# Kernel optimization log

Hardware: AMD Instinct MI355X
Metric: run time of the kernel (lower is better)

The kernel has to match this reference:

```python
import jax, jax.numpy as jnp
import numpy as np

# Module config (matches init_kwargs)
DIM = 256
NUM_HEADS = 8
KS = (7, 7)            # kernel_sizes per split
DIL = (1, 2)           # dilations per split
NUM_SPLITS = 2
HEADS_PER = NUM_HEADS // NUM_SPLITS  # clean partition: 4 heads per split


def _nb_indices(L, ks, dil):
    """NATTEN neighborhood start + relative-position-bias indices along one axis.
    Each residue class (i % dil) is an independent 1D sequence; the k-window is
    clamped (shifted) at the borders exactly as in NATTEN's get_window_start.
    Returns nb [L, ks] key indices and bi [L, ks] rpb indices in [0, 2ks-2].
    """
    i = jnp.arange(L)
    r = i % dil
    p = i // dil
    Lr = (L - r + dil - 1) // dil              # length of residue class
    ps = jnp.clip(p - ks // 2, 0, Lr - ks)     # window start (subsampled coords)
    a = jnp.arange(ks)
    nb = (ps[:, None] + a[None, :]) * dil + r[:, None]   # [L, ks]
    bi = a[None, :] + (ps - p)[:, None] + (ks - 1)       # [L, ks]
    return nb, bi


def _na_split(q, k, v, rpb, ks, dil):
    """natten2dqkrpb -> softmax -> natten2dav for one head-group.
    q pre-scaled. q/k/v: [B,h,H,W,hd], rpb: [h,2ks-1,2ks-1]."""
    H, W = q.shape[2], q.shape[3]
    hn, hb = _nb_indices(H, ks, dil)
    wn, wb = _nb_indices(W, ks, dil)
    # gather local windows: [B,h,H,W,ks,ks,hd]
    kg = k[:, :, hn[:, None, :, None], wn[None, :, None, :], :]
    vg = v[:, :, hn[:, None, :, None], wn[None, :, None, :], :]
    attn = jnp.einsum('bhijd,bhijkld->bhijkl', q, kg)
    attn = attn + rpb[:, hb[:, None, :, None], wb[None, :, None, :]][None]  # [B,h,H,W,ks,ks]
    B, h = attn.shape[0], attn.shape[1]
    attn = jax.nn.softmax(attn.reshape(B, h, H, W, ks * ks), axis=-1)
    attn = attn.reshape(B, h, H, W, ks, ks)
    return jnp.einsum('bhijkl,bhijkld->bhijd', attn, vg)


def _forward(x, w_qkv, b_qkv, w_proj, b_proj, rpb0, rpb1):
    B, H, W, C = x.shape
    hd = C // NUM_HEADS
    scale = hd ** -0.5
    qkv = (x @ w_qkv + b_qkv).reshape(B, H, W, 3, NUM_HEADS, hd)
    qkv = jnp.transpose(qkv, (3, 0, 4, 1, 2, 5))  # [3,B,nh,H,W,hd]
    q, k, v = qkv[0] * scale, qkv[1], qkv[2]
    outs = []
    for s, rpb in enumerate((rpb0, rpb1)):
        sl = slice(s * HEADS_PER, (s + 1) * HEADS_PER)
        outs.append(_na_split(q[:, sl], k[:, sl], v[:, sl], rpb, KS[s], DIL[s]))
    out = jnp.concatenate(outs, axis=1)                      # [B,nh,H,W,hd]
    out = jnp.transpose(out, (0, 2, 3, 1, 4)).reshape(B, H, W, C)
    return out @ w_proj + b_proj


def setup_inputs() -> dict:
    key = jax.random.key(0)
    ks = jax.random.split(key, 6)
    C = DIM
    x = jax.random.normal(ks[0], (2, 56, 56, C), jnp.float32)
    w_qkv = jax.random.normal(ks[1], (C, 3 * C), jnp.float32) * 0.02
    b_qkv = jnp.zeros((3 * C,), jnp.float32)
    w_proj = jax.random.normal(ks[2], (C, C), jnp.float32) * 0.02
    b_proj = jnp.zeros((C,), jnp.float32)
    rpb0 = jax.random.normal(ks[3], (HEADS_PER, 2 * KS[0] - 1, 2 * KS[0] - 1), jnp.float32) * 0.02
    rpb1 = jax.random.normal(ks[4], (HEADS_PER, 2 * KS[1] - 1, 2 * KS[1] - 1), jnp.float32) * 0.02
    return {'x': x, 'w_qkv': w_qkv, 'b_qkv': b_qkv, 'w_proj': w_proj,
            'b_proj': b_proj, 'rpb0': rpb0, 'rpb1': rpb1}


def reference(x, w_qkv, b_qkv, w_proj, b_proj, rpb0, rpb1):
    return _forward(x, w_qkv, b_qkv, w_proj, b_proj, rpb0, rpb1)
```

## Files before the change

### kernel.cpp

```cpp
#include <hip/hip_runtime.h>
#include <stdint.h>

typedef __bf16 bf16_t;
typedef bf16_t bf16x8 __attribute__((ext_vector_type(8)));
typedef float floatx4 __attribute__((ext_vector_type(4)));

#define HW 56
#define NTOK 6272

__device__ __forceinline__ uint16_t f2bf(float f){
  union { float f; uint32_t i; } c; c.f = f;
  uint32_t r = (c.i + 0x7FFFu + ((c.i >> 16) & 1u)) >> 16;
  return (uint16_t)r;
}
__device__ __forceinline__ float bflo(uint32_t u){
  union { uint32_t i; float f; } c; c.i = u << 16; return c.f;
}
__device__ __forceinline__ float bfhi(uint32_t u){
  union { uint32_t i; float f; } c; c.i = u & 0xffff0000u; return c.f;
}

typedef __attribute__((address_space(1))) const void* gptr_t;
typedef __attribute__((address_space(3))) void* lptr_t;

__global__ __launch_bounds__(256) void prep_kernel(
    const float* __restrict__ x,      uint16_t* __restrict__ xb,
    const float* __restrict__ w_qkv,  uint16_t* __restrict__ wqkvT,
    const float* __restrict__ w_proj, uint16_t* __restrict__ wprojT)
{
  __shared__ uint16_t tile[64][65];
  const int bx = blockIdx.x;
  const int t = threadIdx.x;
  if (bx < 784){
    int idx = bx * 256 + t;
    const float4* s = (const float4*)x + (size_t)idx * 2;
    float4 a = s[0], b = s[1];
    uint4 pk;
    pk.x = (uint32_t)f2bf(a.x) | ((uint32_t)f2bf(a.y) << 16);
    pk.y = (uint32_t)f2bf(a.z) | ((uint32_t)f2bf(a.w) << 16);
    pk.z = (uint32_t)f2bf(b.x) | ((uint32_t)f2bf(b.y) << 16);
    pk.w = (uint32_t)f2bf(b.z) | ((uint32_t)f2bf(b.w) << 16);
    ((uint4*)xb)[idx] = pk;
    return;
  }
  const float* src; uint16_t* dst; int N, q;
  if (bx < 832){ q = bx - 784; src = w_qkv;  dst = wqkvT;  N = 768; }
  else         { q = bx - 832; src = w_proj; dst = wprojT; N = 256; }
  const int k0 = (q & 3) * 64, n0 = (q >> 2) * 64;
  for (int idx = t; idx < 64 * 64; idx += 256){
    int r = idx >> 6, c = idx & 63;
    tile[r][c] = f2bf(src[(k0 + r) * N + n0 + c]);
  }
  __syncthreads();
  for (int idx = t; idx < 64 * 64; idx += 256){
    int r = idx >> 6, c = idx & 63;
    dst[(n0 + r) * 256 + k0 + c] = tile[c][r];
  }
}

#define KDIM 256
#define KHALF 128

template<int OUTF32, int AHM, int NT>
__global__ __launch_bounds__(256) void gemm_bt_bias(
    const uint16_t* __restrict__ A,
    const uint16_t* __restrict__ Bt,
    const float* __restrict__ bias,
    void* __restrict__ Cv,
    int N)
{
  constexpr int NF = NT / 32;
  __shared__ __align__(16) uint16_t Al[64 * KHALF];
  __shared__ __align__(16) uint16_t Bl[NT * KHALF];
  const int m0 = blockIdx.x * 64, n0 = blockIdx.y * NT;
  const int t = threadIdx.x;
  const int lane = t & 63;
  const int wave = t >> 6;
  const int wm = (wave & 1) * 32;
  const int wn = (wave >> 1) * (NF * 16);
  const int fr = lane & 15;
  const int q8 = (lane >> 4) * 8;

  floatx4 acc[2][NF];
  #pragma unroll
  for (int mi = 0; mi < 2; mi++)
    #pragma unroll
    for (int nf = 0; nf < NF; nf++) acc[mi][nf] = (floatx4){0.f,0.f,0.f,0.f};

  constexpr int AGRP = 4;
  constexpr int BGRP = NT / 16;

  for (int ko = 0; ko < 2; ko++){
    if (ko) __syncthreads();
    #pragma unroll
    for (int gg = 0; gg < AGRP; gg++){
      int g = wave + gg * 4;
      int L = g * 64 + lane;
      int row = L >> 4, cs = L & 15;
      int cg = cs ^ (row & 15);
      const uint16_t* ga;
      if (AHM){
        int d0 = ko * KHALF + cg * 8;
        ga = A + (size_t)(d0 >> 5) * (NTOK * 32) + (m0 + row) * 32 + (d0 & 31);
      } else {
        ga = A + (size_t)(m0 + row) * KDIM + ko * KHALF + cg * 8;
      }
      __builtin_amdgcn_global_load_lds((gptr_t)ga, (lptr_t)(Al + g * 512), 16, 0, 0);
    }
    #pragma unroll
    for (int gg = 0; gg < BGRP; gg++){
      int g = wave + gg * 4;
      int L = g * 64 + lane;
      int row = L >> 4, cs = L & 15;
      int cg = cs ^ (row & 15);
      const uint16_t* gb = Bt + (size_t)(n0 + row) * KDIM + ko * KHALF + cg * 8;
      __builtin_amdgcn_global_load_lds((gptr_t)gb, (lptr_t)(Bl + g * 512), 16, 0, 0);
    }
    __syncthreads();
    #pragma unroll
    for (int kk = 0; kk < KHALF; kk += 32){
      const int sel = ((((kk >> 3) + (lane >> 4)) ^ fr) << 3);
      bf16x8 a0 = *(const bf16x8*)(Al + (wm + fr)      * KHALF + sel);
      bf16x8 a1 = *(const bf16x8*)(Al + (wm + 16 + fr) * KHALF + sel);
      bf16x8 bfrag[NF];
      #pragma unroll
      for (int nf = 0; nf < NF; nf++)
        bfrag[nf] = *(const bf16x8*)(Bl + (wn + nf * 16 + fr) * KHALF + sel);
      #pragma unroll
      for (int nf = 0; nf < NF; nf++){
        acc[0][nf] = __builtin_amdgcn_mfma_f32_16x16x32_bf16(a0, bfrag[nf], acc[0][nf], 0, 0, 0);
        acc[1][nf] = __builtin_amdgcn_mfma_f32_16x16x32_bf16(a1, bfrag[nf], acc[1][nf], 0, 0, 0);
      }
    }
  }

  const int ccol = lane & 15;
  const int crow = (lane >> 4) * 4;
  float bv[NF];
  #pragma unroll
  for (int nf = 0; nf < NF; nf++) bv[nf] = bias[n0 + wn + nf * 16 + ccol];
  #pragma unroll
  for (int mi = 0; mi < 2; mi++){
    #pragma unroll
    for (int r2 = 0; r2 < 4; r2++){
      int r = m0 + wm + mi * 16 + crow + r2;
      #pragma unroll
      for (int nf = 0; nf < NF; nf++){
        int cidx = r * N + n0 + wn + nf * 16 + ccol;
        if (OUTF32) ((float*)Cv)[cidx] = acc[mi][nf][r2] + bv[nf];
        else        ((uint16_t*)Cv)[cidx] = f2bf(acc[mi][nf][r2] + bv[nf]);
      }
    }
  }
}

#define WIN 20
#define SLP 40

__global__ __launch_bounds__(256, 2) void natten_kernel(
    const uint16_t* __restrict__ qkv,
    const float* __restrict__ rpb0,
    const float* __restrict__ rpb1,
    uint16_t* __restrict__ attnH)
{
  __shared__ uint16_t KS[400 * SLP];
  __shared__ uint16_t VS[400 * SLP];
  __shared__ float RPB[169];

  const int t = threadIdx.x;
  const int z = blockIdx.x;
  const int b = z >> 3, h = z & 7;
  const int j0 = blockIdx.y * 8, i0 = blockIdx.z * 8;
  const int split = h >> 2;
  const int dil = split + 1;
  const float* rpb = (split ? rpb1 : rpb0) + (h & 3) * 169;
  if (t < 169) RPB[t] = rpb[t];

  const int r0 = max(0, i0 - 3 * dil);
  const int c0 = max(0, j0 - 3 * dil);
  const int R  = min(55, i0 + 7 + 3 * dil) - r0 + 1;
  const int C  = min(55, j0 + 7 + 3 * dil) - c0 + 1;

  const int nchunk = R * WIN * 4;
  for (int ch = t; ch < nchunk; ch += 256){
    int tok = ch >> 2, q = ch & 3;
    int tr = tok / WIN;
    int tc = tok - tr * WIN;
    if (tc < C){
      const uint16_t* src = qkv + (size_t)((b * HW + r0 + tr) * HW + c0 + tc) * 768
                            + 256 + h * 32 + q * 8;
      int lds = tok * SLP + q * 8;
      *(bf16x8*)(KS + lds) = *(const bf16x8*)(src);
      *(bf16x8*)(VS + lds) = *(const bf16x8*)(src + 256);
    }
  }
  __syncthreads();

  const int c  = t & 3;
  const int qi = t >> 2;
  const int j = j0 + (qi & 7);
  const int i = i0 + (qi >> 3);

  const int ri = i % dil, pi = i / dil;
  const int rj = j % dil, pj = j / dil;
  const int Lri = (HW - ri + dil - 1) / dil;
  const int Lrj = (HW - rj + dil - 1) / dil;
  const int psi = min(max(pi - 3, 0), Lri - 7);
  const int psj = min(max(pj - 3, 0), Lrj - 7);
  const int bi0 = psi - pi + 6, bj0 = psj - pj + 6;
  const int ni0 = psi * dil + ri, nj0 = psj * dil + rj;

  const int tok = (b * HW + i) * HW + j;
  const float scale = 0.17677669529663687f;

  float qv[8];
  {
    uint4 u = *(const uint4*)(qkv + (size_t)tok * 768 + h * 32 + c * 8);
    qv[0] = bflo(u.x) * scale; qv[1] = bfhi(u.x) * scale;
    qv[2] = bflo(u.y) * scale; qv[3] = bfhi(u.y) * scale;
    qv[4] = bflo(u.z) * scale; qv[5] = bfhi(u.z) * scale;
    qv[6] = bflo(u.w) * scale; qv[7] = bfhi(u.w) * scale;
  }

  const int lbase = (ni0 - r0) * WIN + (nj0 - c0);
  float lgl[13];
  lgl[12] = -1e30f;
  #pragma unroll
  for (int ai = 0; ai < 7; ai++){
    int lrow = lbase + ai * dil * WIN;
    int rpi = (bi0 + ai) * 13 + bj0;
    #pragma unroll
    for (int aj = 0; aj < 7; aj++){
      const int a = ai * 7 + aj;
      uint4 u = *(const uint4*)(KS + (lrow + aj * dil) * SLP + c * 8);
      float d = qv[0] * bflo(u.x) + qv[1] * bfhi(u.x)
              + qv[2] * bflo(u.y) + qv[3] * bfhi(u.y)
              + qv[4] * bflo(u.z) + qv[5] * bfhi(u.z)
              + qv[6] * bflo(u.w) + qv[7] * bfhi(u.w);
      d += __shfl_xor(d, 1);
      d += __shfl_xor(d, 2);
      d += RPB[rpi + aj];
      if ((a & 3) == c) lgl[a >> 2] = d;
    }
  }

  float mx = lgl[0];
  #pragma unroll
  for (int s = 1; s < 13; s++) mx = fmaxf(mx, lgl[s]);
  mx = fmaxf(mx, __shfl_xor(mx, 1));
  mx = fmaxf(mx, __shfl_xor(mx, 2));
  float ssum = 0.f;
  #pragma unroll
  for (int s = 0; s < 13; s++){
    float e = __expf(lgl[s] - mx);
    lgl[s] = e;
    ssum += e;
  }
  ssum += __shfl_xor(ssum, 1);
  ssum += __shfl_xor(ssum, 2);
  float inv = 1.0f / ssum;

  float ov[8];
  #pragma unroll
  for (int d = 0; d < 8; d++) ov[d] = 0.f;

  const int lane4 = t & 60;
  #pragma unroll
  for (int ai = 0; ai < 7; ai++){
    int lrow = lbase + ai * dil * WIN;
    #pragma unroll
    for (int aj = 0; aj < 7; aj++){
      const int a = ai * 7 + aj;
      uint4 u = *(const uint4*)(VS + (lrow + aj * dil) * SLP + c * 8);
      float w = __shfl(lgl[a >> 2], lane4 | (a & 3)) * inv;
      ov[0] += w * bflo(u.x); ov[1] += w * bfhi(u.x);
      ov[2] += w * bflo(u.y); ov[3] += w * bfhi(u.y);
      ov[4] += w * bflo(u.z); ov[5] += w * bfhi(u.z);
      ov[6] += w * bflo(u.w); ov[7] += w * bfhi(u.w);
    }
  }

  uint4 pk;
  pk.x = (uint32_t)f2bf(ov[0]) | ((uint32_t)f2bf(ov[1]) << 16);
  pk.y = (uint32_t)f2bf(ov[2]) | ((uint32_t)f2bf(ov[3]) << 16);
  pk.z = (uint32_t)f2bf(ov[4]) | ((uint32_t)f2bf(ov[5]) << 16);
  pk.w = (uint32_t)f2bf(ov[6]) | ((uint32_t)f2bf(ov[7]) << 16);
  *(uint4*)(attnH + ((size_t)h * NTOK + tok) * 32 + c * 8) = pk;
}

extern "C" void kernel_launch(void* const* d_in, const int* in_sizes, int n_in,
                              void* d_out, int out_size, void* d_ws, size_t ws_size,
                              hipStream_t stream)
{
  (void)in_sizes; (void)n_in; (void)out_size; (void)ws_size;
  const float* x      = (const float*)d_in[0];
  const float* w_qkv  = (const float*)d_in[1];
  const float* b_qkv  = (const float*)d_in[2];
  const float* w_proj = (const float*)d_in[3];
  const float* b_proj = (const float*)d_in[4];
  const float* rpb0   = (const float*)d_in[5];
  const float* rpb1   = (const float*)d_in[6];
  float* out = (float*)d_out;

  uint16_t* wqkvT  = (uint16_t*)d_ws;
  uint16_t* wprojT = wqkvT + 768 * 256;
  uint16_t* xb     = wprojT + 256 * 256;
  uint16_t* qkv    = xb + (size_t)NTOK * 256;
  uint16_t* attn   = qkv + (size_t)NTOK * 768;

  prep_kernel<<<dim3(848), 256, 0, stream>>>(x, xb, w_qkv, wqkvT, w_proj, wprojT);
  gemm_bt_bias<0,0,128><<<dim3(98, 6), 256, 0, stream>>>(xb, wqkvT, b_qkv, qkv, 768);
  natten_kernel<<<dim3(16, 7, 7), 256, 0, stream>>>(qkv, rpb0, rpb1, attn);
  gemm_bt_bias<1,1,64><<<dim3(98, 4), 256, 0, stream>>>(attn, wprojT, b_proj, out, 256);
}
```

Before: 114.7 us.

## Fuse x bf16 conversion into QKV GEMM and repack NATTEN LDS layout

Drops the separate pass that converted x to bf16: the QKV GEMM now loads fp32 x directly, converts it in registers and writes swizzled bf16 into LDS, so the xb round-trip through global memory goes away. The NATTEN kernel stores K/V in LDS as four per-chunk planes with an XOR swizzle in place of padded rows. This cuts LDS use enough to raise the occupancy hint from 2 to 3 blocks per CU. The cost is that the A-tile load in the QKV GEMM becomes a synchronous register path instead of async global_load_lds, and each block re-converts x for every N tile (6 times).

Result: no change. 115.0 us (+0.3%).

```diff
diff --git a/kernel.cpp b/kernel.cpp
--- a/kernel.cpp
+++ b/kernel.cpp
@@ -23,29 +23,17 @@
 typedef __attribute__((address_space(1))) const void* gptr_t;
 typedef __attribute__((address_space(3))) void* lptr_t;
 
-__global__ __launch_bounds__(256) void prep_kernel(
-    const float* __restrict__ x,      uint16_t* __restrict__ xb,
+
+__global__ __launch_bounds__(256) void prep_w_kernel(
     const float* __restrict__ w_qkv,  uint16_t* __restrict__ wqkvT,
     const float* __restrict__ w_proj, uint16_t* __restrict__ wprojT)
 {
   __shared__ uint16_t tile[64][65];
   const int bx = blockIdx.x;
   const int t = threadIdx.x;
-  if (bx < 784){
-    int idx = bx * 256 + t;
-    const float4* s = (const float4*)x + (size_t)idx * 2;
-    float4 a = s[0], b = s[1];
-    uint4 pk;
-    pk.x = (uint32_t)f2bf(a.x) | ((uint32_t)f2bf(a.y) << 16);
-    pk.y = (uint32_t)f2bf(a.z) | ((uint32_t)f2bf(a.w) << 16);
-    pk.z = (uint32_t)f2bf(b.x) | ((uint32_t)f2bf(b.y) << 16);
-    pk.w = (uint32_t)f2bf(b.z) | ((uint32_t)f2bf(b.w) << 16);
-    ((uint4*)xb)[idx] = pk;
-    return;
-  }
   const float* src; uint16_t* dst; int N, q;
-  if (bx < 832){ q = bx - 784; src = w_qkv;  dst = wqkvT;  N = 768; }
-  else         { q = bx - 832; src = w_proj; dst = wprojT; N = 256; }
+  if (bx < 48){ q = bx;      src = w_qkv;  dst = wqkvT;  N = 768; }
+  else        { q = bx - 48; src = w_proj; dst = wprojT; N = 256; }
   const int k0 = (q & 3) * 64, n0 = (q >> 2) * 64;
   for (int idx = t; idx < 64 * 64; idx += 256){
     int r = idx >> 6, c = idx & 63;
@@ -61,9 +49,9 @@
 #define KDIM 256
 #define KHALF 128
 
-template<int OUTF32, int AHM, int NT>
+template<int OUTF32, int AHM, int NT, int AF32>
 __global__ __launch_bounds__(256) void gemm_bt_bias(
-    const uint16_t* __restrict__ A,
+    const void* __restrict__ Av,
     const uint16_t* __restrict__ Bt,
     const float* __restrict__ bias,
     void* __restrict__ Cv,
@@ -79,7 +67,6 @@
   const int wm = (wave & 1) * 32;
   const int wn = (wave >> 1) * (NF * 16);
   const int fr = lane & 15;
-  const int q8 = (lane >> 4) * 8;
 
   floatx4 acc[2][NF];
   #pragma unroll
@@ -92,21 +79,6 @@
 
   for (int ko = 0; ko < 2; ko++){
     if (ko) __syncthreads();
-    #pragma unroll
-    for (int gg = 0; gg < AGRP; gg++){
-      int g = wave + gg * 4;
-      int L = g * 64 + lane;
-      int row = L >> 4, cs = L & 15;
-      int cg = cs ^ (row & 15);
-      const uint16_t* ga;
-      if (AHM){
-        int d0 = ko * KHALF + cg * 8;
-        ga = A + (size_t)(d0 >> 5) * (NTOK * 32) + (m0 + row) * 32 + (d0 & 31);
-      } else {
-        ga = A + (size_t)(m0 + row) * KDIM + ko * KHALF + cg * 8;
-      }
-      __builtin_amdgcn_global_load_lds((gptr_t)ga, (lptr_t)(Al + g * 512), 16, 0, 0);
-    }
     #pragma unroll
     for (int gg = 0; gg < BGRP; gg++){
       int g = wave + gg * 4;
@@ -115,6 +87,32 @@
       int cg = cs ^ (row & 15);
       const uint16_t* gb = Bt + (size_t)(n0 + row) * KDIM + ko * KHALF + cg * 8;
       __builtin_amdgcn_global_load_lds((gptr_t)gb, (lptr_t)(Bl + g * 512), 16, 0, 0);
+    }
+    #pragma unroll
+    for (int gg = 0; gg < AGRP; gg++){
+      int g = wave + gg * 4;
+      int L = g * 64 + lane;
+      int row = L >> 4, cs = L & 15;
+      if (AF32){
+        const float* ga = (const float*)Av + (size_t)(m0 + row) * KDIM + ko * KHALF + cs * 8;
+        float4 f0 = *(const float4*)ga;
+        float4 f1 = *(const float4*)(ga + 4);
+        bf16x8 v;
+        v[0] = (bf16_t)f0.x; v[1] = (bf16_t)f0.y; v[2] = (bf16_t)f0.z; v[3] = (bf16_t)f0.w;
+        v[4] = (bf16_t)f1.x; v[5] = (bf16_t)f1.y; v[6] = (bf16_t)f1.z; v[7] = (bf16_t)f1.w;
+        int slot = row * 16 + (cs ^ (row & 15));
+        *(bf16x8*)(Al + slot * 8) = v;
+      } else {
+        int cg = cs ^ (row & 15);
+        const uint16_t* ga;
+        if (AHM){
+          int d0 = ko * KHALF + cg * 8;
+          ga = (const uint16_t*)Av + (size_t)(d0 >> 5) * (NTOK * 32) + (m0 + row) * 32 + (d0 & 31);
+        } else {
+          ga = (const uint16_t*)Av + (size_t)(m0 + row) * KDIM + ko * KHALF + cg * 8;
+        }
+        __builtin_amdgcn_global_load_lds((gptr_t)ga, (lptr_t)(Al + g * 512), 16, 0, 0);
+      }
     }
     __syncthreads();
     #pragma unroll
@@ -155,16 +153,16 @@
 }
 
 #define WIN 20
-#define SLP 40
-
-__global__ __launch_bounds__(256, 2) void natten_kernel(
+#define PPL 3200
+
+__global__ __launch_bounds__(256, 3) void natten_kernel(
     const uint16_t* __restrict__ qkv,
     const float* __restrict__ rpb0,
     const float* __restrict__ rpb1,
     uint16_t* __restrict__ attnH)
 {
-  __shared__ uint16_t KS[400 * SLP];
-  __shared__ uint16_t VS[400 * SLP];
+  __shared__ uint16_t KS[4 * PPL];
+  __shared__ uint16_t VS[4 * PPL];
   __shared__ float RPB[169];
 
   const int t = threadIdx.x;
@@ -189,7 +187,7 @@
     if (tc < C){
       const uint16_t* src = qkv + (size_t)((b * HW + r0 + tr) * HW + c0 + tc) * 768
                             + 256 + h * 32 + q * 8;
-      int lds = tok * SLP + q * 8;
+      int lds = q * PPL + ((tok ^ ((5 * q) & 7)) << 3);
       *(bf16x8*)(KS + lds) = *(const bf16x8*)(src);
       *(bf16x8*)(VS + lds) = *(const bf16x8*)(src + 256);
     }
@@ -213,6 +211,9 @@
   const int tok = (b * HW + i) * HW + j;
   const float scale = 0.17677669529663687f;
 
+  const int cpl = c * PPL;
+  const int cx  = (5 * c) & 7;
+
   float qv[8];
   {
     uint4 u = *(const uint4*)(qkv + (size_t)tok * 768 + h * 32 + c * 8);
@@ -232,7 +233,8 @@
     #pragma unroll
     for (int aj = 0; aj < 7; aj++){
       const int a = ai * 7 + aj;
-      uint4 u = *(const uint4*)(KS + (lrow + aj * dil) * SLP + c * 8);
+      int tk = lrow + aj * dil;
+      uint4 u = *(const uint4*)(KS + cpl + ((tk ^ cx) << 3));
       float d = qv[0] * bflo(u.x) + qv[1] * bfhi(u.x)
               + qv[2] * bflo(u.y) + qv[3] * bfhi(u.y)
               + qv[4] * bflo(u.z) + qv[5] * bfhi(u.z)
@@ -271,7 +273,8 @@
     #pragma unroll
     for (int aj = 0; aj < 7; aj++){
       const int a = ai * 7 + aj;
-      uint4 u = *(const uint4*)(VS + (lrow + aj * dil) * SLP + c * 8);
+      int tk = lrow + aj * dil;
+      uint4 u = *(const uint4*)(VS + cpl + ((tk ^ cx) << 3));
       float w = __shfl(lgl[a >> 2], lane4 | (a & 3)) * inv;
       ov[0] += w * bflo(u.x); ov[1] += w * bfhi(u.x);
       ov[2] += w * bflo(u.y); ov[3] += w * bfhi(u.y);
@@ -304,12 +307,11 @@
 
   uint16_t* wqkvT  = (uint16_t*)d_ws;
   uint16_t* wprojT = wqkvT + 768 * 256;
-  uint16_t* xb     = wprojT + 256 * 256;
-  uint16_t* qkv    = xb + (size_t)NTOK * 256;
+  uint16_t* qkv    = wprojT + 256 * 256;
   uint16_t* attn   = qkv + (size_t)NTOK * 768;
 
-  prep_kernel<<<dim3(848), 256, 0, stream>>>(x, xb, w_qkv, wqkvT, w_proj, wprojT);
-  gemm_bt_bias<0,0,128><<<dim3(98, 6), 256, 0, stream>>>(xb, wqkvT, b_qkv, qkv, 768);
+  prep_w_kernel<<<dim3(64), 256, 0, stream>>>(w_qkv, wqkvT, w_proj, wprojT);
+  gemm_bt_bias<0, 0, 128, 1><<<dim3(98, 6), 256, 0, stream>>>(x, wqkvT, b_qkv, qkv, 768);
   natten_kernel<<<dim3(16, 7, 7), 256, 0, stream>>>(qkv, rpb0, rpb1, attn);
-  gemm_bt_bias<1,1,64><<<dim3(98, 4), 256, 0, stream>>>(attn, wprojT, b_proj, out, 256);
-}
+  gemm_bt_bias<1, 1, 64, 0><<<dim3(98, 4), 256, 0, stream>>>(attn, wprojT, b_proj, out, 256);
+}
```

## Restructure NATTEN QK to per-lane full-dim dot2 with swizzled unpadded LDS

Applied to the files above, without the earlier changes.

The QK stage is reorganised so each of the four lanes per query computes whole 32-dim dot products for its own subset of the 49 neighbours, using bf16 dot2 instructions. This removes the cross-lane shuffle reductions and the per-element bf16-to-float conversions. K and V shared-memory tiles lose their padding and use XOR swizzles instead, with V split into per-quarter planes, which shrinks LDS so the launch bound can allow three blocks per CU. The cost is four 16-byte K loads per neighbour per lane, more registers for the full query vector, and possible bank conflicts if a swizzle misses a pattern.

Result: faster. 103.4 us (median of 2 runs) (-9.9%).

```diff
diff --git a/kernel.cpp b/kernel.cpp
--- a/kernel.cpp
+++ b/kernel.cpp
@@ -3,6 +3,7 @@
 
 typedef __bf16 bf16_t;
 typedef bf16_t bf16x8 __attribute__((ext_vector_type(8)));
+typedef bf16_t bf16x2 __attribute__((ext_vector_type(2)));
 typedef float floatx4 __attribute__((ext_vector_type(4)));
 
 #define HW 56
@@ -20,8 +21,19 @@
   union { uint32_t i; float f; } c; c.i = u & 0xffff0000u; return c.f;
 }
 
+__device__ __forceinline__ float bdot2(uint32_t ka, uint32_t qa, float acc){
+#if __has_builtin(__builtin_amdgcn_fdot2_f32_bf16)
+  union { uint32_t u; bf16x2 v; } A, B;
+  A.u = ka; B.u = qa;
+  return __builtin_amdgcn_fdot2_f32_bf16(A.v, B.v, acc, false);
+#else
+  return acc + bflo(ka) * bflo(qa) + bfhi(ka) * bfhi(qa);
+#endif
+}
+
 typedef __attribute__((address_space(1))) const void* gptr_t;
 typedef __attribute__((address_space(3))) void* lptr_t;
+
 
 __global__ __launch_bounds__(256) void prep_kernel(
     const float* __restrict__ x,      uint16_t* __restrict__ xb,
@@ -79,7 +91,6 @@
   const int wm = (wave & 1) * 32;
   const int wn = (wave >> 1) * (NF * 16);
   const int fr = lane & 15;
-  const int q8 = (lane >> 4) * 8;
 
   floatx4 acc[2][NF];
   #pragma unroll
@@ -155,16 +166,16 @@
 }
 
 #define WIN 20
-#define SLP 40
-
-__global__ __launch_bounds__(256, 2) void natten_kernel(
+#define PPL 3200
+
+__global__ __launch_bounds__(256, 3) void natten_kernel(
     const uint16_t* __restrict__ qkv,
     const float* __restrict__ rpb0,
     const float* __restrict__ rpb1,
     uint16_t* __restrict__ attnH)
 {
-  __shared__ uint16_t KS[400 * SLP];
-  __shared__ uint16_t VS[400 * SLP];
+  __shared__ uint16_t KS[400 * 32];
+  __shared__ uint16_t VS[4 * PPL];
   __shared__ float RPB[169];
 
   const int t = threadIdx.x;
@@ -189,9 +200,10 @@
     if (tc < C){
       const uint16_t* src = qkv + (size_t)((b * HW + r0 + tr) * HW + c0 + tc) * 768
                             + 256 + h * 32 + q * 8;
-      int lds = tok * SLP + q * 8;
-      *(bf16x8*)(KS + lds) = *(const bf16x8*)(src);
-      *(bf16x8*)(VS + lds) = *(const bf16x8*)(src + 256);
+      int kl = tok * 32 + ((q ^ (tok & 3) ^ ((tok >> 2) & 3)) << 3);
+      *(bf16x8*)(KS + kl) = *(const bf16x8*)(src);
+      int vl = q * PPL + ((tok ^ ((5 * q) & 7)) << 3);
+      *(bf16x8*)(VS + vl) = *(const bf16x8*)(src + 256);
     }
   }
   __syncthreads();
@@ -213,35 +225,42 @@
   const int tok = (b * HW + i) * HW + j;
   const float scale = 0.17677669529663687f;
 
-  float qv[8];
+  uint32_t qp[16];
   {
-    uint4 u = *(const uint4*)(qkv + (size_t)tok * 768 + h * 32 + c * 8);
-    qv[0] = bflo(u.x) * scale; qv[1] = bfhi(u.x) * scale;
-    qv[2] = bflo(u.y) * scale; qv[3] = bfhi(u.y) * scale;
-    qv[4] = bflo(u.z) * scale; qv[5] = bfhi(u.z) * scale;
-    qv[6] = bflo(u.w) * scale; qv[7] = bfhi(u.w) * scale;
+    const uint16_t* qsrc = qkv + (size_t)tok * 768 + h * 32;
+    uint4 u0 = *(const uint4*)(qsrc);
+    uint4 u1 = *(const uint4*)(qsrc + 8);
+    uint4 u2 = *(const uint4*)(qsrc + 16);
+    uint4 u3 = *(const uint4*)(qsrc + 24);
+    qp[0]  = u0.x; qp[1]  = u0.y; qp[2]  = u0.z; qp[3]  = u0.w;
+    qp[4]  = u1.x; qp[5]  = u1.y; qp[6]  = u1.z; qp[7]  = u1.w;
+    qp[8]  = u2.x; qp[9]  = u2.y; qp[10] = u2.z; qp[11] = u2.w;
+    qp[12] = u3.x; qp[13] = u3.y; qp[14] = u3.z; qp[15] = u3.w;
   }
 
   const int lbase = (ni0 - r0) * WIN + (nj0 - c0);
+
   float lgl[13];
-  lgl[12] = -1e30f;
-  #pragma unroll
-  for (int ai = 0; ai < 7; ai++){
-    int lrow = lbase + ai * dil * WIN;
-    int rpi = (bi0 + ai) * 13 + bj0;
-    #pragma unroll
-    for (int aj = 0; aj < 7; aj++){
-      const int a = ai * 7 + aj;
-      uint4 u = *(const uint4*)(KS + (lrow + aj * dil) * SLP + c * 8);
-      float d = qv[0] * bflo(u.x) + qv[1] * bfhi(u.x)
-              + qv[2] * bflo(u.y) + qv[3] * bfhi(u.y)
-              + qv[4] * bflo(u.z) + qv[5] * bfhi(u.z)
-              + qv[6] * bflo(u.w) + qv[7] * bfhi(u.w);
-      d += __shfl_xor(d, 1);
-      d += __shfl_xor(d, 2);
-      d += RPB[rpi + aj];
-      if ((a & 3) == c) lgl[a >> 2] = d;
-    }
+  #pragma unroll
+  for (int m = 0; m < 13; m++){
+    int a = 4 * m + c;
+    const bool valid = (a <= 48);
+    if (!valid) a = 48;
+    int ai = a / 7;
+    int aj = a - ai * 7;
+    int tk = lbase + (ai * WIN + aj) * dil;
+    const int tswz = ((tk & 3) ^ ((tk >> 2) & 3));
+    float dacc = 0.f;
+    #pragma unroll
+    for (int cc = 0; cc < 4; cc++){
+      uint4 u = *(const uint4*)(KS + tk * 32 + ((cc ^ tswz) << 3));
+      dacc = bdot2(u.x, qp[cc * 4 + 0], dacc);
+      dacc = bdot2(u.y, qp[cc * 4 + 1], dacc);
+      dacc = bdot2(u.z, qp[cc * 4 + 2], dacc);
+      dacc = bdot2(u.w, qp[cc * 4 + 3], dacc);
+    }
+    float d = dacc * scale + RPB[(bi0 + ai) * 13 + (bj0 + aj)];
+    lgl[m] = valid ? d : -1e30f;
   }
 
   float mx = lgl[0];
@@ -264,6 +283,8 @@
   #pragma unroll
   for (int d = 0; d < 8; d++) ov[d] = 0.f;
 
+  const int cpl = c * PPL;
+  const int cx  = (5 * c) & 7;
   const int lane4 = t & 60;
   #pragma unroll
   for (int ai = 0; ai < 7; ai++){
@@ -271,7 +292,8 @@
     #pragma unroll
     for (int aj = 0; aj < 7; aj++){
       const int a = ai * 7 + aj;
-      uint4 u = *(const uint4*)(VS + (lrow + aj * dil) * SLP + c * 8);
+      int tk = lrow + aj * dil;
+      uint4 u = *(const uint4*)(VS + cpl + ((tk ^ cx) << 3));
       float w = __shfl(lgl[a >> 2], lane4 | (a & 3)) * inv;
       ov[0] += w * bflo(u.x); ov[1] += w * bfhi(u.x);
       ov[2] += w * bflo(u.y); ov[3] += w * bfhi(u.y);
@@ -309,7 +331,7 @@
   uint16_t* attn   = qkv + (size_t)NTOK * 768;
 
   prep_kernel<<<dim3(848), 256, 0, stream>>>(x, xb, w_qkv, wqkvT, w_proj, wprojT);
-  gemm_bt_bias<0,0,128><<<dim3(98, 6), 256, 0, stream>>>(xb, wqkvT, b_qkv, qkv, 768);
+  gemm_bt_bias<0, 0, 128><<<dim3(98, 6), 256, 0, stream>>>(xb, wqkvT, b_qkv, qkv, 768);
   natten_kernel<<<dim3(16, 7, 7), 256, 0, stream>>>(qkv, rpb0, rpb1, attn);
-  gemm_bt_bias<1,1,64><<<dim3(98, 4), 256, 0, stream>>>(attn, wprojT, b_proj, out, 256);
-}
+  gemm_bt_bias<1, 1, 64><<<dim3(98, 4), 256, 0, stream>>>(attn, wprojT, b_proj, out, 256);
+}
```
